# Optimization experiments

Hardware: AMD Instinct MI355X
Metric: run time of the kernel (lower is better)

## Reference

```python
import jax, jax.numpy as jnp
import numpy as np

N, E, IN, HID, H, G = 50000, 400000, 128, 16, 11, 64
HC = HID * H  # 176
OUT, NC = 32, 10
EPS = 1e-5


def setup_inputs() -> dict:
    key = jax.random.key(0)
    ks = jax.random.split(key, 20)
    def n(i, shape, s=0.05):
        return jax.random.normal(ks[i], shape, jnp.float32) * s
    inp = {}
    inp["x"] = jax.random.normal(ks[0], (N, IN), jnp.float32)
    inp["edge_index"] = jax.random.randint(ks[1], (2, E), 0, N, dtype=jnp.int32)
    inp["batch"] = jnp.sort(jax.random.randint(ks[2], (N,), 0, G, dtype=jnp.int32))
    inp["W_pre"] = n(3, (IN, HC)); inp["b_pre"] = jnp.zeros((HC,), jnp.float32)
    # GraphNorm params for gn_pre, gn1..gn4 stacked: [5, HC]
    inp["gn_w"] = jnp.ones((5, HC), jnp.float32)
    inp["gn_b"] = jnp.zeros((5, HC), jnp.float32)
    inp["gn_ms"] = jnp.ones((5, HC), jnp.float32)  # mean_scale
    # conv1..conv4 (concat=True) stacked params
    inp["conv_Wl"] = n(4, (4, HC, HC)); inp["conv_Wr"] = n(5, (4, HC, HC))
    inp["conv_att"] = n(6, (4, H, HID))
    inp["conv_b"] = jnp.zeros((4, HC), jnp.float32)
    inp["conv_Wres"] = n(7, (4, HC, HC))
    # conv5 (concat=False -> out dim HID)
    inp["c5_Wl"] = n(8, (HC, HC)); inp["c5_Wr"] = n(9, (HC, HC))
    inp["c5_att"] = n(10, (H, HID))
    inp["c5_b"] = jnp.zeros((HID,), jnp.float32)
    inp["c5_Wres"] = n(11, (HC, HID))
    inp["W_o1"] = n(12, (HID, HID)); inp["b_o1"] = jnp.zeros((HID,), jnp.float32)
    inp["W_o2"] = n(13, (HID, OUT)); inp["b_o2"] = jnp.zeros((OUT,), jnp.float32)
    inp["W_cls"] = n(14, (OUT, NC)); inp["b_cls"] = jnp.zeros((NC,), jnp.float32)
    return inp


def graph_norm(x, w, b, ms, batch, cnt):
    # PyG GraphNorm: out = w * (x - ms*mean) / sqrt(var + eps) + b, stats per graph
    mean = jax.ops.segment_sum(x, batch, G) / cnt  # [G, F]
    xc = x - mean[batch] * ms
    var = jax.ops.segment_sum(xc * xc, batch, G) / cnt
    std = jnp.sqrt(var + EPS)
    return w * xc / std[batch] + b


def gatv2_conv(x, Wl, Wr, att, bias, Wres, src, dst, concat):
    # src/dst already include self-loops (PyG add_self_loops=True)
    xl = (x @ Wl).reshape(N, H, -1)  # source transform [N,H,C]
    xr = (x @ Wr).reshape(N, H, -1)  # target transform [N,H,C]
    e = jax.nn.leaky_relu(xl[src] + xr[dst], 0.2)          # [E',H,C]
    alpha = jnp.einsum('ehc,hc->eh', e, att)               # [E',H]
    amax = jax.ops.segment_max(alpha, dst, N)
    amax = jnp.where(jnp.isfinite(amax), amax, 0.0)
    ex = jnp.exp(alpha - amax[dst])
    den = jax.ops.segment_sum(ex, dst, N)
    a = ex / (den[dst] + 1e-16)
    out = jax.ops.segment_sum(xl[src] * a[..., None], dst, N)  # [N,H,C]
    out = out.reshape(N, -1) if concat else out.mean(axis=1)
    return out + x @ Wres + bias


def reference(x, edge_index, batch, W_pre, b_pre, gn_w, gn_b, gn_ms,
              conv_Wl, conv_Wr, conv_att, conv_b, conv_Wres,
              c5_Wl, c5_Wr, c5_att, c5_b, c5_Wres,
              W_o1, b_o1, W_o2, b_o2, W_cls, b_cls):
    loops = jnp.arange(N, dtype=edge_index.dtype)
    src = jnp.concatenate([edge_index[0], loops])
    dst = jnp.concatenate([edge_index[1], loops])
    cnt = jax.ops.segment_sum(jnp.ones((N, 1), jnp.float32), batch, G)
    cnt = jnp.maximum(cnt, 1.0)  # guard empty graphs

    h = x @ W_pre + b_pre
    h = graph_norm(h, gn_w[0], gn_b[0], gn_ms[0], batch, cnt)
    h = jax.nn.relu(h)
    for i in range(4):
        h = gatv2_conv(h, conv_Wl[i], conv_Wr[i], conv_att[i], conv_b[i],
                       conv_Wres[i], src, dst, concat=True)
        h = graph_norm(h, gn_w[i + 1], gn_b[i + 1], gn_ms[i + 1], batch, cnt)
        h = jax.nn.relu(h)
    h = gatv2_conv(h, c5_Wl, c5_Wr, c5_att, c5_b, c5_Wres, src, dst, concat=False)
    h = jax.nn.relu(h)
    h = jax.nn.relu(h @ W_o1 + b_o1)
    h = jax.nn.relu(h @ W_o2 + b_o2)
    return h @ W_cls + b_cls
```

## Files before the change

### kernel.cpp

```cpp
#include <hip/hip_runtime.h>
#include <math.h>

#define N_NODES 50000
#define N_EDGES 400000
#define IN_F 128
#define HC 176
#define NGRAPH 64
#define NBLK_ATTN 12500
#define NCHUNK 16

typedef _Float16 half8 __attribute__((ext_vector_type(8)));
typedef float floatx4 __attribute__((ext_vector_type(4)));

#define PREH 45056
#define MATH 67584
#define TOT_PAIRS 495616
#define KCBYTES 22528
#define GX8 49

__global__ void prep_kernel(const float* __restrict__ Wpre,
                            const float* __restrict__ cWl, const float* __restrict__ cWr,
                            const float* __restrict__ cWres,
                            const float* __restrict__ c5Wl, const float* __restrict__ c5Wr,
                            _Float16* __restrict__ wp) {
  int gid = blockIdx.x * 256 + threadIdx.x;
  if (gid >= TOT_PAIRS) return;
  int mat, idx;
  if (gid < 22528) { mat = 0; idx = gid; }
  else { int g = gid - 22528; mat = 1 + g / 33792; idx = g % 33792; }
  int kc = idx / 5632;
  int rem = idx - kc * 5632;
  int ct = rem / 512;
  int li = rem - ct * 512;
  int lane = li >> 3, j = li & 7;
  int k = kc * 32 + ((lane >> 4) << 3) + j;
  int col = ct * 16 + (lane & 15);
  const float* src; int Ksrc; size_t base;
  if (mat == 0) { src = Wpre; Ksrc = 128; base = 0; }
  else if (mat <= 12) {
    int lm = mat - 1; int layer = lm / 3; int sub = lm - layer * 3;
    const float* s = (sub == 0) ? cWl : (sub == 1) ? cWr : cWres;
    src = s + (size_t)layer * HC * HC; Ksrc = HC;
    base = PREH + (size_t)lm * MATH;
  } else {
    src = (mat == 13) ? c5Wl : c5Wr; Ksrc = HC;
    base = PREH + (size_t)12 * MATH + (size_t)(mat - 13) * MATH;
  }
  float v = (k < Ksrc) ? src[(size_t)k * HC + col] : 0.0f;
  _Float16 h = (_Float16)v;
  _Float16 l = (_Float16)(v - (float)h);
  size_t o = base + (size_t)(kc * 11 + ct) * 1024 + li;
  wp[o] = h;
  wp[o + 512] = l;
}

__global__ __launch_bounds__(256, 2) void gemm_mfma(
    const float* __restrict__ A, int M, int K, int nkc, int nmat,
    const _Float16* __restrict__ Wp, int matStride,
    const float* __restrict__ scsh, const int* __restrict__ batch,
    const float* __restrict__ bias0, const float* __restrict__ bias1,
    const float* __restrict__ bias2,
    float* __restrict__ out0, float* __restrict__ out1, float* __restrict__ out2) {
  __shared__ __align__(16) char smem[2 * KCBYTES];
  const int b = blockIdx.x;
  const int grp = b >> 3, sub = b & 7;
  const int mat = grp % nmat;
  const int tile = ((grp / nmat) << 3) | sub;
  if (tile * 128 >= M) return;
  const _Float16* W = Wp + (size_t)mat * matStride;
  float* outp = (mat == 0) ? out0 : (mat == 1) ? out1 : out2;
  const float* bias = (mat == 0) ? bias0 : (mat == 1) ? bias1 : bias2;
  const int tid = threadIdx.x;
  const int lane = tid & 63;
  const int wv = tid >> 6;
  const int m16 = lane & 15, quad = lane >> 4;
  const int kb = quad << 3;
  const int rowBase = tile * 128 + wv * 32;
  const int rA0 = min(rowBase + m16, M - 1);
  const int rA1 = min(rowBase + 16 + m16, M - 1);
  const float* ap0 = A + (size_t)rA0 * K + kb;
  const float* ap1 = A + (size_t)rA1 * K + kb;
  const float* sc0 = nullptr; const float* sh0 = nullptr;
  const float* sc1 = nullptr; const float* sh1 = nullptr;
  if (scsh) {
    int g0 = batch[rA0], g1 = batch[rA1];
    sc0 = scsh + (size_t)g0 * HC + kb;
    sh0 = scsh + (size_t)(NGRAPH + g0) * HC + kb;
    sc1 = scsh + (size_t)g1 * HC + kb;
    sh1 = scsh + (size_t)(NGRAPH + g1) * HC + kb;
  }

  auto stage = [&](int kc, int buf) {
    const char* src = (const char*)W + (size_t)kc * KCBYTES;
    char* dst = smem + buf * KCBYTES;
#pragma unroll
    for (int i = 0; i < 6; i++) {
      int idx = wv * 6 + i;
      if (idx < 22) {
        __builtin_amdgcn_global_load_lds(
            (const __attribute__((address_space(1))) unsigned int*)(src + idx * 1024 + lane * 16),
            (__attribute__((address_space(3))) unsigned int*)(dst + idx * 1024),
            16, 0, 0);
      }
    }
  };

  floatx4 acc0[11], acc1[11];
#pragma unroll
  for (int ct = 0; ct < 11; ct++)
#pragma unroll
    for (int r = 0; r < 4; r++) { acc0[ct][r] = 0.0f; acc1[ct][r] = 0.0f; }

  stage(0, 0);

  for (int kc = 0; kc < nkc; kc++) {
    const int buf = kc & 1;
    __syncthreads();
    if (kc + 1 < nkc) stage(kc + 1, 1 - buf);

    const int koff = kc << 5;
    float va0[8], va1[8];
    if (koff + kb + 8 <= K) {
      float4 u0 = *(const float4*)(ap0 + koff);
      float4 u1 = *(const float4*)(ap0 + koff + 4);
      float4 w0 = *(const float4*)(ap1 + koff);
      float4 w1 = *(const float4*)(ap1 + koff + 4);
      va0[0] = u0.x; va0[1] = u0.y; va0[2] = u0.z; va0[3] = u0.w;
      va0[4] = u1.x; va0[5] = u1.y; va0[6] = u1.z; va0[7] = u1.w;
      va1[0] = w0.x; va1[1] = w0.y; va1[2] = w0.z; va1[3] = w0.w;
      va1[4] = w1.x; va1[5] = w1.y; va1[6] = w1.z; va1[7] = w1.w;
      if (scsh) {
        float s0[8], h0[8], s1[8], h1[8];
        float4 t;
        t = *(const float4*)(sc0 + koff);     s0[0]=t.x; s0[1]=t.y; s0[2]=t.z; s0[3]=t.w;
        t = *(const float4*)(sc0 + koff + 4); s0[4]=t.x; s0[5]=t.y; s0[6]=t.z; s0[7]=t.w;
        t = *(const float4*)(sh0 + koff);     h0[0]=t.x; h0[1]=t.y; h0[2]=t.z; h0[3]=t.w;
        t = *(const float4*)(sh0 + koff + 4); h0[4]=t.x; h0[5]=t.y; h0[6]=t.z; h0[7]=t.w;
        t = *(const float4*)(sc1 + koff);     s1[0]=t.x; s1[1]=t.y; s1[2]=t.z; s1[3]=t.w;
        t = *(const float4*)(sc1 + koff + 4); s1[4]=t.x; s1[5]=t.y; s1[6]=t.z; s1[7]=t.w;
        t = *(const float4*)(sh1 + koff);     h1[0]=t.x; h1[1]=t.y; h1[2]=t.z; h1[3]=t.w;
        t = *(const float4*)(sh1 + koff + 4); h1[4]=t.x; h1[5]=t.y; h1[6]=t.z; h1[7]=t.w;
#pragma unroll
        for (int j = 0; j < 8; j++) {
          va0[j] = fmaxf(fmaf(va0[j], s0[j], h0[j]), 0.0f);
          va1[j] = fmaxf(fmaf(va1[j], s1[j], h1[j]), 0.0f);
        }
      }
    } else {
#pragma unroll
      for (int j = 0; j < 8; j++) { va0[j] = 0.0f; va1[j] = 0.0f; }
    }
    half8 ah0, al0, ah1, al1;
#pragma unroll
    for (int j = 0; j < 8; j++) {
      _Float16 h = (_Float16)va0[j];
      ah0[j] = h; al0[j] = (_Float16)(va0[j] - (float)h);
      _Float16 g = (_Float16)va1[j];
      ah1[j] = g; al1[j] = (_Float16)(va1[j] - (float)g);
    }
    const char* bbase = smem + buf * KCBYTES + lane * 16;
#pragma unroll
    for (int ct = 0; ct < 11; ct++) {
      half8 bh = *(const half8*)(bbase + ct * 2048);
      half8 bl = *(const half8*)(bbase + ct * 2048 + 1024);
      acc0[ct] = __builtin_amdgcn_mfma_f32_16x16x32_f16(ah0, bh, acc0[ct], 0, 0, 0);
      acc1[ct] = __builtin_amdgcn_mfma_f32_16x16x32_f16(ah1, bh, acc1[ct], 0, 0, 0);
      acc0[ct] = __builtin_amdgcn_mfma_f32_16x16x32_f16(al0, bh, acc0[ct], 0, 0, 0);
      acc1[ct] = __builtin_amdgcn_mfma_f32_16x16x32_f16(al1, bh, acc1[ct], 0, 0, 0);
      acc0[ct] = __builtin_amdgcn_mfma_f32_16x16x32_f16(ah0, bl, acc0[ct], 0, 0, 0);
      acc1[ct] = __builtin_amdgcn_mfma_f32_16x16x32_f16(ah1, bl, acc1[ct], 0, 0, 0);
    }
  }

  float bv[11];
#pragma unroll
  for (int ct = 0; ct < 11; ct++) bv[ct] = bias ? bias[ct * 16 + m16] : 0.0f;
#pragma unroll
  for (int r = 0; r < 4; r++) {
    int row0 = rowBase + (quad << 2) + r;
    if (row0 < M) {
      float* op = outp + (size_t)row0 * HC + m16;
#pragma unroll
      for (int ct = 0; ct < 11; ct++) op[ct * 16] = acc0[ct][r] + bv[ct];
    }
    int row1 = row0 + 16;
    if (row1 < M) {
      float* op = outp + (size_t)row1 * HC + m16;
#pragma unroll
      for (int ct = 0; ct < 11; ct++) op[ct * 16] = acc1[ct][r] + bv[ct];
    }
  }
}

__global__ __launch_bounds__(256) void gn_stats_kernel(const float* __restrict__ h,
                                                       const int* __restrict__ batch,
                                                       float* __restrict__ stats) {
  int t = threadIdx.x;
  int wv = t >> 6, lane = t & 63;
  if (lane >= 44) return;
  int n0 = blockIdx.x * 64 + wv * 16;
  if (n0 >= N_NODES) return;
  int n1 = min(n0 + 16, N_NODES);
  int f4 = lane * 4;
  float4 s = make_float4(0.f, 0.f, 0.f, 0.f);
  float4 ss = make_float4(0.f, 0.f, 0.f, 0.f);
  int gcur = batch[n0];
  for (int n = n0; n < n1; n++) {
    int g = batch[n];
    if (g != gcur) {
      float* sp = stats + (size_t)gcur * HC + f4;
      float* qp = stats + (size_t)(NGRAPH + gcur) * HC + f4;
      atomicAdd(sp + 0, s.x); atomicAdd(sp + 1, s.y);
      atomicAdd(sp + 2, s.z); atomicAdd(sp + 3, s.w);
      atomicAdd(qp + 0, ss.x); atomicAdd(qp + 1, ss.y);
      atomicAdd(qp + 2, ss.z); atomicAdd(qp + 3, ss.w);
      s = make_float4(0.f, 0.f, 0.f, 0.f);
      ss = make_float4(0.f, 0.f, 0.f, 0.f);
      gcur = g;
    }
    float4 v = *(const float4*)(h + (size_t)n * HC + f4);
    s.x += v.x; s.y += v.y; s.z += v.z; s.w += v.w;
    ss.x = fmaf(v.x, v.x, ss.x); ss.y = fmaf(v.y, v.y, ss.y);
    ss.z = fmaf(v.z, v.z, ss.z); ss.w = fmaf(v.w, v.w, ss.w);
  }
  float* sp = stats + (size_t)gcur * HC + f4;
  float* qp = stats + (size_t)(NGRAPH + gcur) * HC + f4;
  atomicAdd(sp + 0, s.x); atomicAdd(sp + 1, s.y);
  atomicAdd(sp + 2, s.z); atomicAdd(sp + 3, s.w);
  atomicAdd(qp + 0, ss.x); atomicAdd(qp + 1, ss.y);
  atomicAdd(qp + 2, ss.z); atomicAdd(qp + 3, ss.w);
}

__global__ __launch_bounds__(256) void part_reduce_kernel(
    const float* __restrict__ parts, const float* __restrict__ partq,
    const int* __restrict__ gstart, float* __restrict__ stats) {
  int idx = blockIdx.x * 256 + threadIdx.x;
  if (idx >= NGRAPH * NCHUNK * HC) return;
  int f = idx % HC;
  int gc = idx / HC;
  int g = gc / NCHUNK, c = gc % NCHUNK;
  int s0 = gstart[g], s1 = gstart[g + 1];
  int b0 = (s0 + 3) >> 2, b1 = (s1 + 3) >> 2;
  int len = b1 - b0;
  if (len <= 0) return;
  int per = (len + NCHUNK - 1) / NCHUNK;
  int cb0 = b0 + c * per;
  int cb1 = min(cb0 + per, b1);
  if (cb0 >= cb1) return;
  float s = 0.f, ss = 0.f;
  for (int b = cb0; b < cb1; b++) {
    s += parts[(size_t)b * HC + f];
    ss += partq[(size_t)b * HC + f];
  }
  atomicAdd(&stats[g * HC + f], s);
  atomicAdd(&stats[(NGRAPH + g) * HC + f], ss);
}

__global__ void gn_finalize_kernel(const float* __restrict__ stats, const int* __restrict__ cntInt,
                                   const float* __restrict__ gnw, const float* __restrict__ gnb,
                                   const float* __restrict__ gnms, int row,
                                   float* __restrict__ scsh) {
  int i = blockIdx.x * 256 + threadIdx.x;
  if (i >= NGRAPH * HC) return;
  int g = i / HC, f = i - g * HC;
  float c = fmaxf((float)cntInt[g], 1.0f);
  float m = stats[i] / c;
  float sq = stats[NGRAPH * HC + i] / c;
  float ms = gnms[row * HC + f];
  float var = sq - m * m * ms * (2.0f - ms);
  float w = gnw[row * HC + f], b = gnb[row * HC + f];
  float scale = w / sqrtf(var + 1e-5f);
  float shift = b - scale * ms * m;
  scsh[i] = scale;
  scsh[NGRAPH * HC + i] = shift;
}

__global__ void cnt_bsearch_kernel(const int* __restrict__ batch, int* __restrict__ cntInt,
                                   int* __restrict__ gstart) {
  int g = threadIdx.x;
  if (g >= NGRAPH) return;
  auto lb = [&](int v) {
    int lo = 0, hi = N_NODES;
    while (lo < hi) {
      int mid = (lo + hi) >> 1;
      if (batch[mid] < v) lo = mid + 1; else hi = mid;
    }
    return lo;
  };
  int a = lb(g), b = lb(g + 1);
  cntInt[g] = b - a;
  gstart[g] = a;
  if (g == NGRAPH - 1) gstart[NGRAPH] = N_NODES;
}

__global__ void deg_hist_kernel(const int* __restrict__ dstE, int* __restrict__ deg) {
  int e = blockIdx.x * 256 + threadIdx.x;
  if (e < N_EDGES) atomicAdd(&deg[dstE[e]], 1);
}

__global__ void scan1_kernel(const int* __restrict__ deg, int* __restrict__ bsum) {
  __shared__ int sd[256];
  int i = blockIdx.x * 256 + threadIdx.x;
  sd[threadIdx.x] = (i < N_NODES) ? deg[i] : 0;
  __syncthreads();
  for (int s = 128; s > 0; s >>= 1) {
    if (threadIdx.x < s) sd[threadIdx.x] += sd[threadIdx.x + s];
    __syncthreads();
  }
  if (threadIdx.x == 0) bsum[blockIdx.x] = sd[0];
}

__global__ void scan2_kernel(int* __restrict__ bsum, int nb) {
  __shared__ int sd[256];
  int t = threadIdx.x;
  int v0 = (t < nb) ? bsum[t] : 0;
  sd[t] = v0;
  __syncthreads();
  for (int s = 1; s < 256; s <<= 1) {
    int v = (t >= s) ? sd[t - s] : 0;
    __syncthreads();
    sd[t] += v;
    __syncthreads();
  }
  if (t < nb) bsum[t] = sd[t] - v0;
}

__global__ void scan3_kernel(const int* __restrict__ deg, const int* __restrict__ bsum,
                             int* __restrict__ rowptr) {
  __shared__ int sd[256];
  int i = blockIdx.x * 256 + threadIdx.x;
  int t = threadIdx.x;
  int d = (i < N_NODES) ? deg[i] : 0;
  sd[t] = d;
  __syncthreads();
  for (int s = 1; s < 256; s <<= 1) {
    int v = (t >= s) ? sd[t - s] : 0;
    __syncthreads();
    sd[t] += v;
    __syncthreads();
  }
  if (i < N_NODES) rowptr[i] = bsum[blockIdx.x] + sd[t] - d;
  if (i == 0) rowptr[N_NODES] = N_EDGES;
}

__global__ void scatter_kernel(const int* __restrict__ srcE, const int* __restrict__ dstE,
                               const int* __restrict__ rowptr, int* __restrict__ fill,
                               int* __restrict__ colA) {
  int e = blockIdx.x * 256 + threadIdx.x;
  if (e < N_EDGES) {
    int d = dstE[e];
    int pos = rowptr[d] + atomicAdd(&fill[d], 1);
    colA[pos] = srcE[e];
  }
}

#define AEDGE(V, D, ACC)                                                      \
  do {                                                                        \
    float e0 = (V).x + xrv.x; e0 = fmaxf(e0, 0.2f * e0);                      \
    float e1 = (V).y + xrv.y; e1 = fmaxf(e1, 0.2f * e1);                      \
    float e2 = (V).z + xrv.z; e2 = fmaxf(e2, 0.2f * e2);                      \
    float e3 = (V).w + xrv.w; e3 = fmaxf(e3, 0.2f * e3);                      \
    float p = fmaf(e3, av.w, fmaf(e2, av.z, fmaf(e1, av.y, e0 * av.x)));      \
    p += __shfl_xor(p, 1);                                                    \
    p += __shfl_xor(p, 2);                                                    \
    float pp = __expf(p);                                                     \
    (D) += pp;                                                                \
    (ACC).x = fmaf(pp, (V).x, (ACC).x);                                       \
    (ACC).y = fmaf(pp, (V).y, (ACC).y);                                       \
    (ACC).z = fmaf(pp, (V).z, (ACC).z);                                       \
    (ACC).w = fmaf(pp, (V).w, (ACC).w);                                       \
  } while (0)

__global__ __launch_bounds__(256) void attn_concat_kernel(
    const float* __restrict__ xl, const float* __restrict__ xr,
    const float* __restrict__ att, const int* __restrict__ rowptr,
    const int* __restrict__ colA, float* __restrict__ out,
    const int* __restrict__ batch, float* __restrict__ stats,
    float* __restrict__ parts, float* __restrict__ partq) {
  __shared__ float sv[4 * HC];
  int t = threadIdx.x;
  int node = blockIdx.x * 4 + (t >> 6);
  int lane = t & 63;
  if (lane < 44) {
    const float4 av = *(const float4*)(att + lane * 4);
    size_t base = (size_t)node * HC + lane * 4;
    const float4 xrv = *(const float4*)(xr + base);
    int start = rowptr[node], end = rowptr[node + 1];
    float d = 0.0f, dB = 0.0f;
    float4 acc = make_float4(0.f, 0.f, 0.f, 0.f);
    float4 accB = make_float4(0.f, 0.f, 0.f, 0.f);
    float4 p1, p2;
    if (start < end)     p1 = *(const float4*)(xl + (size_t)colA[start] * HC + lane * 4);
    if (start + 1 < end) p2 = *(const float4*)(xl + (size_t)colA[start + 1] * HC + lane * 4);
    {
      float4 svv = *(const float4*)(xl + base);
      AEDGE(svv, d, acc);
    }
    int j = start;
    for (; j + 3 < end; j += 2) {
      float4 n1 = *(const float4*)(xl + (size_t)colA[j + 2] * HC + lane * 4);
      float4 n2 = *(const float4*)(xl + (size_t)colA[j + 3] * HC + lane * 4);
      AEDGE(p1, d, acc);
      AEDGE(p2, dB, accB);
      p1 = n1; p2 = n2;
    }
    if (j < end)     AEDGE(p1, d, acc);
    if (j + 1 < end) AEDGE(p2, dB, accB);
    if (j + 2 < end) {
      float4 n1 = *(const float4*)(xl + (size_t)colA[j + 2] * HC + lane * 4);
      AEDGE(n1, d, acc);
    }
    d += dB;
    acc.x += accB.x; acc.y += accB.y; acc.z += accB.z; acc.w += accB.w;
    float rd = 1.0f / (d + 1e-16f);
    float4 o = *(const float4*)(out + base);
    o.x = fmaf(acc.x, rd, o.x);
    o.y = fmaf(acc.y, rd, o.y);
    o.z = fmaf(acc.z, rd, o.z);
    o.w = fmaf(acc.w, rd, o.w);
    *(float4*)(out + base) = o;
    *(float4*)(&sv[(t >> 6) * HC + lane * 4]) = o;
  }
  __syncthreads();
  if (t < HC) {
    int b = blockIdx.x;
    int g0 = batch[b * 4];
    float s = 0.0f, ss = 0.0f;
#pragma unroll
    for (int w = 0; w < 4; w++) {
      int g = batch[b * 4 + w];
      float v = sv[w * HC + t];
      if (g == g0) {
        s += v;
        ss = fmaf(v, v, ss);
      } else {
        atomicAdd(&stats[g * HC + t], v);
        atomicAdd(&stats[(NGRAPH + g) * HC + t], v * v);
      }
    }
    parts[(size_t)b * HC + t] = s;
    partq[(size_t)b * HC + t] = ss;
  }
}

__global__ __launch_bounds__(256) void attn_mean_kernel(
    const float* __restrict__ xl, const float* __restrict__ xr,
    const float* __restrict__ att, const int* __restrict__ rowptr,
    const int* __restrict__ colA, const float* __restrict__ res16,
    float* __restrict__ out16) {
  int t = threadIdx.x;
  int node = blockIdx.x * 4 + (t >> 6);
  int lane = t & 63;
  if (node >= N_NODES) return;
  int L = (lane < 44) ? lane : 0;
  const float4 av = *(const float4*)(att + L * 4);
  size_t base = (size_t)node * HC + L * 4;
  const float4 xrv = *(const float4*)(xr + base);
  int start = rowptr[node], end = rowptr[node + 1];
  float d = 0.0f, dB = 0.0f;
  float4 acc = make_float4(0.f, 0.f, 0.f, 0.f);
  float4 accB = make_float4(0.f, 0.f, 0.f, 0.f);
  float4 p1, p2;
  if (start < end)     p1 = *(const float4*)(xl + (size_t)colA[start] * HC + L * 4);
  if (start + 1 < end) p2 = *(const float4*)(xl + (size_t)colA[start + 1] * HC + L * 4);
  {
    float4 sv = *(const float4*)(xl + base);
    AEDGE(sv, d, acc);
  }
  int j = start;
  for (; j + 3 < end; j += 2) {
    float4 n1 = *(const float4*)(xl + (size_t)colA[j + 2] * HC + L * 4);
    float4 n2 = *(const float4*)(xl + (size_t)colA[j + 3] * HC + L * 4);
    AEDGE(p1, d, acc);
    AEDGE(p2, dB, accB);
    p1 = n1; p2 = n2;
  }
  if (j < end)     AEDGE(p1, d, acc);
  if (j + 1 < end) AEDGE(p2, dB, accB);
  if (j + 2 < end) {
    float4 n1 = *(const float4*)(xl + (size_t)colA[j + 2] * HC + L * 4);
    AEDGE(n1, d, acc);
  }
  d += dB;
  acc.x += accB.x; acc.y += accB.y; acc.z += accB.z; acc.w += accB.w;
  float rd = 1.0f / (d + 1e-16f);
  float4 o;
  o.x = (lane < 44) ? acc.x * rd : 0.0f;
  o.y = (lane < 44) ? acc.y * rd : 0.0f;
  o.z = (lane < 44) ? acc.z * rd : 0.0f;
  o.w = (lane < 44) ? acc.w * rd : 0.0f;
#pragma unroll
  for (int w = 4; w <= 32; w <<= 1) {
    o.x += __shfl_xor(o.x, w);
    o.y += __shfl_xor(o.y, w);
    o.z += __shfl_xor(o.z, w);
    o.w += __shfl_xor(o.w, w);
  }
  if (lane < 4) {
    const float* rp = res16 + (size_t)node * 16 + lane * 4;
    float4 r = *(const float4*)rp;
    float4 ov;
    ov.x = fmaxf(fmaf(o.x, 1.0f / 11.0f, r.x), 0.0f);
    ov.y = fmaxf(fmaf(o.y, 1.0f / 11.0f, r.y), 0.0f);
    ov.z = fmaxf(fmaf(o.z, 1.0f / 11.0f, r.z), 0.0f);
    ov.w = fmaxf(fmaf(o.w, 1.0f / 11.0f, r.w), 0.0f);
    *(float4*)(out16 + (size_t)node * 16 + lane * 4) = ov;
  }
}

__global__ __launch_bounds__(256) void res16_kernel(const float* __restrict__ h,
                                                    const float* __restrict__ scsh,
                                                    const int* __restrict__ batch,
                                                    const float* __restrict__ Wres,
                                                    const float* __restrict__ b16,
                                                    float* __restrict__ res16) {
  __shared__ float Ws[176 * 16];
  __shared__ float hs[16 * 176];
  int t = threadIdx.x;
  for (int i = t; i < 176 * 16; i += 256) Ws[i] = Wres[i];
  int n0 = blockIdx.x * 16;
  for (int i = t; i < 16 * 176; i += 256) {
    int row = i / 176, k = i - row * 176;
    int g = batch[n0 + row];
    float v = h[(size_t)n0 * HC + i];
    hs[i] = fmaxf(fmaf(v, scsh[g * HC + k], scsh[(NGRAPH + g) * HC + k]), 0.0f);
  }
  __syncthreads();
  int tx = t & 15, ty = t >> 4;
  float acc = b16[tx];
  for (int k = 0; k < HC; k++) acc = fmaf(hs[ty * HC + k], Ws[k * 16 + tx], acc);
  res16[(size_t)(n0 + ty) * 16 + tx] = acc;
}

__global__ __launch_bounds__(256) void head_kernel(
    const float* __restrict__ in16, const float* __restrict__ Wo1,
    const float* __restrict__ bo1, const float* __restrict__ Wo2,
    const float* __restrict__ bo2, const float* __restrict__ Wc,
    const float* __restrict__ bc, float* __restrict__ outp) {
  __shared__ float w1[256], w2[512], wcS[320], b1[16], b2[32], bcS[10];
  int t = threadIdx.x;
  for (int i = t; i < 256; i += 256) w1[i] = Wo1[i];
  for (int i = t; i < 512; i += 256) w2[i] = Wo2[i];
  for (int i = t; i < 320; i += 256) wcS[i] = Wc[i];
  if (t < 16) b1[t] = bo1[t];
  if (t < 32) b2[t] = bo2[t];
  if (t < 10) bcS[t] = bc[t];
  __syncthreads();
  int n = blockIdx.x * 256 + t;
  if (n >= N_NODES) return;
  float x[16];
#pragma unroll
  for (int i = 0; i < 16; i++) x[i] = in16[(size_t)n * 16 + i];
  float o1[16];
#pragma unroll
  for (int j = 0; j < 16; j++) {
    float a = b1[j];
#pragma unroll
    for (int k = 0; k < 16; k++) a = fmaf(x[k], w1[k * 16 + j], a);
    o1[j] = fmaxf(a, 0.0f);
  }
  float o2[32];
#pragma unroll
  for (int j = 0; j < 32; j++) {
    float a = b2[j];
#pragma unroll
    for (int k = 0; k < 16; k++) a = fmaf(o1[k], w2[k * 32 + j], a);
    o2[j] = fmaxf(a, 0.0f);
  }
#pragma unroll
  for (int j = 0; j < 10; j++) {
    float a = bcS[j];
#pragma unroll
    for (int k = 0; k < 32; k++) a = fmaf(o2[k], wcS[k * 10 + j], a);
    outp[(size_t)n * 10 + j] = a;
  }
}

extern "C" void kernel_launch(void* const* d_in, const int* in_sizes, int n_in,
                              void* d_out, int out_size, void* d_ws, size_t ws_size,
                              hipStream_t stream) {
  (void)in_sizes; (void)n_in; (void)out_size; (void)ws_size;
  const float* x     = (const float*)d_in[0];
  const int*   ei    = (const int*)d_in[1];
  const int*   srcE  = ei;
  const int*   dstE  = ei + N_EDGES;
  const int*   batch = (const int*)d_in[2];
  const float* W_pre = (const float*)d_in[3];
  const float* b_pre = (const float*)d_in[4];
  const float* gn_w  = (const float*)d_in[5];
  const float* gn_b  = (const float*)d_in[6];
  const float* gn_ms = (const float*)d_in[7];
  const float* cWl   = (const float*)d_in[8];
  const float* cWr   = (const float*)d_in[9];
  const float* cAtt  = (const float*)d_in[10];
  const float* cB    = (const float*)d_in[11];
  const float* cWres = (const float*)d_in[12];
  const float* c5Wl  = (const float*)d_in[13];
  const float* c5Wr  = (const float*)d_in[14];
  const float* c5Att = (const float*)d_in[15];
  const float* c5b   = (const float*)d_in[16];
  const float* c5Wres= (const float*)d_in[17];
  const float* Wo1   = (const float*)d_in[18];
  const float* bo1   = (const float*)d_in[19];
  const float* Wo2   = (const float*)d_in[20];
  const float* bo2   = (const float*)d_in[21];
  const float* Wc    = (const float*)d_in[22];
  const float* bc    = (const float*)d_in[23];

  const size_t FB = (size_t)N_NODES * HC;
  const size_t STB = (size_t)2 * NGRAPH * HC;
  const size_t PB = (size_t)NBLK_ATTN * HC;
  float* ws    = (float*)d_ws;
  float* buf0  = ws;
  float* buf1  = ws + FB;
  float* buf2  = ws + 2 * FB;
  float* buf3  = ws + 3 * FB;
  float* res16 = ws + 4 * FB;
  float* out16 = res16 + (size_t)N_NODES * 16;
  float* stats = out16 + (size_t)N_NODES * 16;
  float* scsh  = stats + 5 * STB;
  float* parts = scsh + STB;
  float* partq = parts + PB;
  _Float16* wph = (_Float16*)(partq + PB);
  int* ibase   = (int*)((char*)wph + (size_t)991232 * 2);
  int* cntInt  = ibase;
  int* gstart  = ibase + 64;
  int* deg     = gstart + 65;
  int* fill    = deg + N_NODES;
  int* rowptr  = fill + N_NODES;
  int* colA    = rowptr + N_NODES + 1;
  int* bsum    = colA + N_EDGES;

  const int NB = (N_NODES + 255) / 256;

  hipMemsetAsync(deg, 0, sizeof(int) * 2 * N_NODES, stream);
  hipMemsetAsync(stats, 0, sizeof(float) * 5 * STB, stream);

  prep_kernel<<<(TOT_PAIRS + 255) / 256, 256, 0, stream>>>(W_pre, cWl, cWr, cWres, c5Wl, c5Wr, wph);
  cnt_bsearch_kernel<<<1, 64, 0, stream>>>(batch, cntInt, gstart);
  deg_hist_kernel<<<(N_EDGES + 255) / 256, 256, 0, stream>>>(dstE, deg);
  scan1_kernel<<<NB, 256, 0, stream>>>(deg, bsum);
  scan2_kernel<<<1, 256, 0, stream>>>(bsum, NB);
  scan3_kernel<<<NB, 256, 0, stream>>>(deg, bsum, rowptr);
  scatter_kernel<<<(N_EDGES + 255) / 256, 256, 0, stream>>>(srcE, dstE, rowptr, fill, colA);

  const int GNB = (N_NODES + 63) / 64;
  const int PRB = (NGRAPH * NCHUNK * HC + 255) / 256;

  gemm_mfma<<<GX8 * 1 * 8, 256, 0, stream>>>(x, N_NODES, IN_F, 4, 1, wph, 0,
                                             nullptr, nullptr,
                                             b_pre, nullptr, nullptr,
                                             buf0, nullptr, nullptr);
  gn_stats_kernel<<<GNB, 256, 0, stream>>>(buf0, batch, stats);
  gn_finalize_kernel<<<(NGRAPH * HC + 255) / 256, 256, 0, stream>>>(stats, cntInt, gn_w, gn_b, gn_ms, 0, scsh);

  float* h = buf0;
  float* o = buf3;
  for (int i = 0; i < 4; i++) {
    const _Float16* Wcat_i = wph + PREH + (size_t)(3 * i) * MATH;
    gemm_mfma<<<GX8 * 3 * 8, 256, 0, stream>>>(h, N_NODES, HC, 6, 3, Wcat_i, MATH,
                                               scsh, batch,
                                               nullptr, nullptr, cB + i * HC,
                                               buf1, buf2, o);
    float* st = stats + (size_t)(i + 1) * STB;
    attn_concat_kernel<<<NBLK_ATTN, 256, 0, stream>>>(buf1, buf2, cAtt + i * HC,
                                                      rowptr, colA, o, batch, st,
                                                      parts, partq);
    part_reduce_kernel<<<PRB, 256, 0, stream>>>(parts, partq, gstart, st);
    gn_finalize_kernel<<<(NGRAPH * HC + 255) / 256, 256, 0, stream>>>(st, cntInt, gn_w, gn_b, gn_ms, i + 1, scsh);
    float* tmp = h; h = o; o = tmp;
  }

  const _Float16* Wc5 = wph + PREH + (size_t)12 * MATH;
  gemm_mfma<<<GX8 * 2 * 8, 256, 0, stream>>>(h, N_NODES, HC, 6, 2, Wc5, MATH,
                                             scsh, batch,
                                             nullptr, nullptr, nullptr,
                                             buf1, buf2, nullptr);
  res16_kernel<<<N_NODES / 16, 256, 0, stream>>>(h, scsh, batch, c5Wres, c5b, res16);
  attn_mean_kernel<<<(N_NODES + 3) / 4, 256, 0, stream>>>(buf1, buf2, c5Att, rowptr, colA, res16, out16);

  head_kernel<<<NB, 256, 0, stream>>>(out16, Wo1, bo1, Wo2, bo2, Wc, bc, (float*)d_out);
}
```

Baseline: 798.2 us.

## Fuse GraphNorm stats into pre-GEMM epilogue, raise GEMM occupancy, merge memsets

The separate gn_stats pass over the pre-projection output is replaced by per-tile partial sums computed in the GEMM epilogue. The epilogue reduces through shared memory, writes per-tile partials for the tile's first graph, and adds rows from a second graph into the stats with atomics. The partials then go through the existing part_reduce kernel, which now takes a rows-per-block parameter. Separately, the conv GEMMs use launch bounds asking for 3 waves per SIMD instead of 2, and deg/fill are moved next to stats so one memset clears both. The stats path assumes a 128-row tile spans at most two graphs, and the higher occupancy target may cause register spills.

```diff
diff --git a/kernel.cpp b/kernel.cpp
--- a/kernel.cpp
+++ b/kernel.cpp
@@ -54,13 +54,15 @@
   wp[o + 512] = l;
 }
 
-__global__ __launch_bounds__(256, 2) void gemm_mfma(
+template <int MINW, bool DOSTATS>
+__global__ __launch_bounds__(256, MINW) void gemm_mfma_t(
     const float* __restrict__ A, int M, int K, int nkc, int nmat,
     const _Float16* __restrict__ Wp, int matStride,
     const float* __restrict__ scsh, const int* __restrict__ batch,
     const float* __restrict__ bias0, const float* __restrict__ bias1,
     const float* __restrict__ bias2,
-    float* __restrict__ out0, float* __restrict__ out1, float* __restrict__ out2) {
+    float* __restrict__ out0, float* __restrict__ out1, float* __restrict__ out2,
+    float* __restrict__ parts, float* __restrict__ partq, float* __restrict__ stats) {
   __shared__ __align__(16) char smem[2 * KCBYTES];
   const int b = blockIdx.x;
   const int grp = b >> 3, sub = b & 7;
@@ -190,57 +192,78 @@
       for (int ct = 0; ct < 11; ct++) op[ct * 16] = acc1[ct][r] + bv[ct];
     }
   }
-}
-
-__global__ __launch_bounds__(256) void gn_stats_kernel(const float* __restrict__ h,
-                                                       const int* __restrict__ batch,
-                                                       float* __restrict__ stats) {
-  int t = threadIdx.x;
-  int wv = t >> 6, lane = t & 63;
-  if (lane >= 44) return;
-  int n0 = blockIdx.x * 64 + wv * 16;
-  if (n0 >= N_NODES) return;
-  int n1 = min(n0 + 16, N_NODES);
-  int f4 = lane * 4;
-  float4 s = make_float4(0.f, 0.f, 0.f, 0.f);
-  float4 ss = make_float4(0.f, 0.f, 0.f, 0.f);
-  int gcur = batch[n0];
-  for (int n = n0; n < n1; n++) {
-    int g = batch[n];
-    if (g != gcur) {
-      float* sp = stats + (size_t)gcur * HC + f4;
-      float* qp = stats + (size_t)(NGRAPH + gcur) * HC + f4;
-      atomicAdd(sp + 0, s.x); atomicAdd(sp + 1, s.y);
-      atomicAdd(sp + 2, s.z); atomicAdd(sp + 3, s.w);
-      atomicAdd(qp + 0, ss.x); atomicAdd(qp + 1, ss.y);
-      atomicAdd(qp + 2, ss.z); atomicAdd(qp + 3, ss.w);
-      s = make_float4(0.f, 0.f, 0.f, 0.f);
-      ss = make_float4(0.f, 0.f, 0.f, 0.f);
-      gcur = g;
-    }
-    float4 v = *(const float4*)(h + (size_t)n * HC + f4);
-    s.x += v.x; s.y += v.y; s.z += v.z; s.w += v.w;
-    ss.x = fmaf(v.x, v.x, ss.x); ss.y = fmaf(v.y, v.y, ss.y);
-    ss.z = fmaf(v.z, v.z, ss.z); ss.w = fmaf(v.w, v.w, ss.w);
-  }
-  float* sp = stats + (size_t)gcur * HC + f4;
-  float* qp = stats + (size_t)(NGRAPH + gcur) * HC + f4;
-  atomicAdd(sp + 0, s.x); atomicAdd(sp + 1, s.y);
-  atomicAdd(sp + 2, s.z); atomicAdd(sp + 3, s.w);
-  atomicAdd(qp + 0, ss.x); atomicAdd(qp + 1, ss.y);
-  atomicAdd(qp + 2, ss.z); atomicAdd(qp + 3, ss.w);
+
+  if (DOSTATS) {
+    int gTile = batch[tile * 128];
+    int lastRow = min(tile * 128 + 127, M - 1);
+    bool straddle = (batch[lastRow] != gTile);
+    bool validR[8]; bool otherR[8];
+#pragma unroll
+    for (int r = 0; r < 4; r++) {
+      int row0 = rowBase + (quad << 2) + r;
+      validR[r] = (row0 < M);
+      otherR[r] = validR[r] && (batch[min(row0, M - 1)] != gTile);
+      int row1 = row0 + 16;
+      validR[4 + r] = (row1 < M);
+      otherR[4 + r] = validR[4 + r] && (batch[min(row1, M - 1)] != gTile);
+    }
+    __syncthreads();
+    float* red = (float*)smem;
+#pragma unroll
+    for (int ct = 0; ct < 11; ct++) {
+      float sA = 0.f, qA = 0.f, sB = 0.f, qB = 0.f;
+#pragma unroll
+      for (int r = 0; r < 4; r++) {
+        if (validR[r]) {
+          float v = acc0[ct][r] + bv[ct];
+          if (otherR[r]) { sB += v; qB = fmaf(v, v, qB); }
+          else           { sA += v; qA = fmaf(v, v, qA); }
+        }
+        if (validR[4 + r]) {
+          float v = acc1[ct][r] + bv[ct];
+          if (otherR[4 + r]) { sB += v; qB = fmaf(v, v, qB); }
+          else               { sA += v; qA = fmaf(v, v, qA); }
+        }
+      }
+      sA += __shfl_xor(sA, 16); sA += __shfl_xor(sA, 32);
+      qA += __shfl_xor(qA, 16); qA += __shfl_xor(qA, 32);
+      sB += __shfl_xor(sB, 16); sB += __shfl_xor(sB, 32);
+      qB += __shfl_xor(qB, 16); qB += __shfl_xor(qB, 32);
+      if (quad == 0) {
+        float* slot = red + (((wv * 11 + ct) * 16 + m16) << 2);
+        slot[0] = sA; slot[1] = qA; slot[2] = sB; slot[3] = qB;
+      }
+    }
+    __syncthreads();
+    if (tid < HC) {
+      int col = tid;
+      float sA = 0.f, qA = 0.f, sB = 0.f, qB = 0.f;
+#pragma unroll
+      for (int w = 0; w < 4; w++) {
+        float* slot = red + (((w * 11 + col / 16) * 16 + (col & 15)) << 2);
+        sA += slot[0]; qA += slot[1]; sB += slot[2]; qB += slot[3];
+      }
+      parts[(size_t)tile * HC + col] = sA;
+      partq[(size_t)tile * HC + col] = qA;
+      if (straddle) {
+        int g2 = batch[lastRow];
+        atomicAdd(&stats[g2 * HC + col], sB);
+        atomicAdd(&stats[(NGRAPH + g2) * HC + col], qB);
+      }
+    }
+  }
 }
 
 __global__ __launch_bounds__(256) void part_reduce_kernel(
     const float* __restrict__ parts, const float* __restrict__ partq,
-    const int* __restrict__ gstart, float* __restrict__ stats) {
+    const int* __restrict__ gstart, float* __restrict__ stats, int rpb) {
   int idx = blockIdx.x * 256 + threadIdx.x;
   if (idx >= NGRAPH * NCHUNK * HC) return;
   int f = idx % HC;
   int gc = idx / HC;
   int g = gc / NCHUNK, c = gc % NCHUNK;
   int s0 = gstart[g], s1 = gstart[g + 1];
-  int b0 = (s0 + 3) >> 2, b1 = (s1 + 3) >> 2;
+  int b0 = (s0 + rpb - 1) / rpb, b1 = (s1 + rpb - 1) / rpb;
   int len = b1 - b0;
   if (len <= 0) return;
   int per = (len + NCHUNK - 1) / NCHUNK;
@@ -618,23 +641,22 @@
   float* res16 = ws + 4 * FB;
   float* out16 = res16 + (size_t)N_NODES * 16;
   float* stats = out16 + (size_t)N_NODES * 16;
-  float* scsh  = stats + 5 * STB;
+  int* deg     = (int*)(stats + 5 * STB);
+  int* fill    = deg + N_NODES;
+  float* scsh  = (float*)(fill + N_NODES);
   float* parts = scsh + STB;
   float* partq = parts + PB;
   _Float16* wph = (_Float16*)(partq + PB);
   int* ibase   = (int*)((char*)wph + (size_t)991232 * 2);
   int* cntInt  = ibase;
   int* gstart  = ibase + 64;
-  int* deg     = gstart + 65;
-  int* fill    = deg + N_NODES;
-  int* rowptr  = fill + N_NODES;
+  int* rowptr  = gstart + 65;
   int* colA    = rowptr + N_NODES + 1;
   int* bsum    = colA + N_EDGES;
 
   const int NB = (N_NODES + 255) / 256;
 
-  hipMemsetAsync(deg, 0, sizeof(int) * 2 * N_NODES, stream);
-  hipMemsetAsync(stats, 0, sizeof(float) * 5 * STB, stream);
+  hipMemsetAsync(stats, 0, sizeof(float) * 5 * STB + sizeof(int) * 2 * N_NODES, stream);
 
   prep_kernel<<<(TOT_PAIRS + 255) / 256, 256, 0, stream>>>(W_pre, cWl, cWr, cWres, c5Wl, c5Wr, wph);
   cnt_bsearch_kernel<<<1, 64, 0, stream>>>(batch, cntInt, gstart);
@@ -644,38 +666,37 @@
   scan3_kernel<<<NB, 256, 0, stream>>>(deg, bsum, rowptr);
   scatter_kernel<<<(N_EDGES + 255) / 256, 256, 0, stream>>>(srcE, dstE, rowptr, fill, colA);
 
-  const int GNB = (N_NODES + 63) / 64;
   const int PRB = (NGRAPH * NCHUNK * HC + 255) / 256;
 
-  gemm_mfma<<<GX8 * 1 * 8, 256, 0, stream>>>(x, N_NODES, IN_F, 4, 1, wph, 0,
-                                             nullptr, nullptr,
-                                             b_pre, nullptr, nullptr,
-                                             buf0, nullptr, nullptr);
-  gn_stats_kernel<<<GNB, 256, 0, stream>>>(buf0, batch, stats);
+  gemm_mfma_t<2, true><<<GX8 * 1 * 8, 256, 0, stream>>>(
+      x, N_NODES, IN_F, 4, 1, wph, 0, nullptr, batch,
+      b_pre, nullptr, nullptr, buf0, nullptr, nullptr,
+      parts, partq, stats);
+  part_reduce_kernel<<<PRB, 256, 0, stream>>>(parts, partq, gstart, stats, 128);
   gn_finalize_kernel<<<(NGRAPH * HC + 255) / 256, 256, 0, stream>>>(stats, cntInt, gn_w, gn_b, gn_ms, 0, scsh);
 
   float* h = buf0;
   float* o = buf3;
   for (int i = 0; i < 4; i++) {
     const _Float16* Wcat_i = wph + PREH + (size_t)(3 * i) * MATH;
-    gemm_mfma<<<GX8 * 3 * 8, 256, 0, stream>>>(h, N_NODES, HC, 6, 3, Wcat_i, MATH,
-                                               scsh, batch,
-                                               nullptr, nullptr, cB + i * HC,
-                                               buf1, buf2, o);
+    gemm_mfma_t<3, false><<<GX8 * 3 * 8, 256, 0, stream>>>(
+        h, N_NODES, HC, 6, 3, Wcat_i, MATH, scsh, batch,
+        nullptr, nullptr, cB + i * HC, buf1, buf2, o,
+        nullptr, nullptr, nullptr);
     float* st = stats + (size_t)(i + 1) * STB;
     attn_concat_kernel<<<NBLK_ATTN, 256, 0, stream>>>(buf1, buf2, cAtt + i * HC,
                                                       rowptr, colA, o, batch, st,
                                                       parts, partq);
-    part_reduce_kernel<<<PRB, 256, 0, stream>>>(parts, partq, gstart, st);
+    part_reduce_kernel<<<PRB, 256, 0, stream>>>(parts, partq, gstart, st, 4);
     gn_finalize_kernel<<<(NGRAPH * HC + 255) / 256, 256, 0, stream>>>(st, cntInt, gn_w, gn_b, gn_ms, i + 1, scsh);
     float* tmp = h; h = o; o = tmp;
   }
 
   const _Float16* Wc5 = wph + PREH + (size_t)12 * MATH;
-  gemm_mfma<<<GX8 * 2 * 8, 256, 0, stream>>>(h, N_NODES, HC, 6, 2, Wc5, MATH,
-                                             scsh, batch,
-                                             nullptr, nullptr, nullptr,
-                                             buf1, buf2, nullptr);
+  gemm_mfma_t<3, false><<<GX8 * 2 * 8, 256, 0, stream>>>(
+      h, N_NODES, HC, 6, 2, Wc5, MATH, scsh, batch,
+      nullptr, nullptr, nullptr, buf1, buf2, nullptr,
+      nullptr, nullptr, nullptr);
   res16_kernel<<<N_NODES / 16, 256, 0, stream>>>(h, scsh, batch, c5Wres, c5b, res16);
   attn_mean_kernel<<<(N_NODES + 3) / 4, 256, 0, stream>>>(buf1, buf2, c5Att, rowptr, colA, res16, out16);
 
```

Measured after the change: 764.0 us. 1.04x faster.
